# Kernel tuning notes

Measured on AMD Instinct MI355X. Metric: run time of the kernel, lower is better.

## Reference

```python
import jax, jax.numpy as jnp
import numpy as np
from jax import lax

NUM_QUBITS = 4
NUM_LAYERS = 2
EPS = 1e-5  # BatchNorm eps; eval mode with running_mean=0, running_var=1


def _cnot_ring_matrix():
    # CNOT(0,1); CNOT(1,2); CNOT(2,3); CNOT(3,0) as one 16x16 permutation.
    # PennyLane convention: wire 0 is the most-significant bit of the basis index.
    M = np.zeros((16, 16), dtype=np.complex64)
    for b in range(16):
        bb = b
        for cw, tw in [(0, 1), (1, 2), (2, 3), (3, 0)]:
            if (bb >> (3 - cw)) & 1:
                bb ^= 1 << (3 - tw)
        M[bb, b] = 1.0
    return M

CNOT_RING = jnp.asarray(_cnot_ring_matrix())
# ZSIGNS[w, b] = <b|Z_w|b> = +/-1
ZSIGNS = jnp.asarray(np.array([[1.0 - 2.0 * ((b >> (3 - w)) & 1) for b in range(16)]
                               for w in range(NUM_QUBITS)], dtype=np.float32))


def conv_bn_relu(x, w, b, gamma, beta):
    # Conv2d(k=3, pad=1) + BatchNorm2d (eval: mean=0, var=1) + ReLU, NCHW
    x = lax.conv_general_dilated(x, w, (1, 1), ((1, 1), (1, 1)),
                                 dimension_numbers=('NCHW', 'OIHW', 'NCHW'))
    x = x + b[None, :, None, None]
    x = gamma[None, :, None, None] * x * (1.0 / np.sqrt(1.0 + EPS)) + beta[None, :, None, None]
    return jax.nn.relu(x)


def maxpool2(x):
    return lax.reduce_window(x, -jnp.inf, lax.max, (1, 1, 2, 2), (1, 1, 2, 2), 'VALID')


def avgpool2(x):
    return lax.reduce_window(x, 0.0, lax.add, (1, 1, 2, 2), (1, 1, 2, 2), 'VALID') * 0.25


def quantum_layer(x, weights):
    # x: [B, 16] softmax outputs. Amplitude-encode (abs + L2 normalize), then
    # BasicEntanglerLayers (RX rotations + CNOT ring) x NUM_LAYERS, then <Z_i>.
    psi = jnp.abs(x)
    psi = psi / jnp.linalg.norm(psi, axis=1, keepdims=True)
    psi = psi.astype(jnp.complex64)  # [B, 16] batched statevectors
    for l in range(NUM_LAYERS):
        c = jnp.cos(weights[l] * 0.5).astype(jnp.complex64)
        s = jnp.sin(weights[l] * 0.5).astype(jnp.complex64)
        U = jnp.ones((1, 1), dtype=jnp.complex64)
        for q in range(NUM_QUBITS):
            g = jnp.stack([jnp.stack([c[q], -1j * s[q]]),
                           jnp.stack([-1j * s[q], c[q]])])  # RX(theta_q)
            U = jnp.kron(U, g)
        U = CNOT_RING @ U  # rotations first, then entangling ring
        psi = psi @ U.T    # batched apply: [B,16] x [16,16]
    probs = jnp.real(psi * jnp.conj(psi))  # [B, 16]
    return probs @ ZSIGNS.T                # [B, 4] Pauli-Z expvals


def setup_inputs() -> dict:
    key = jax.random.key(0)
    ks = jax.random.split(key, 16)
    B = 1024
    f32 = jnp.float32

    def w(k, shape, fan_in):
        return jax.random.normal(k, shape, dtype=f32) * np.float32(1.0 / np.sqrt(fan_in))

    inp = {
        'x': jax.random.normal(ks[0], (B, 3, 32, 32), dtype=f32),
        'conv1_w': w(ks[1], (32, 3, 3, 3), 3 * 9), 'conv1_b': jnp.zeros((32,), f32),
        'bn1_g': jnp.ones((32,), f32), 'bn1_b': jnp.zeros((32,), f32),
        'conv2_w': w(ks[2], (64, 32, 3, 3), 32 * 9), 'conv2_b': jnp.zeros((64,), f32),
        'bn2_g': jnp.ones((64,), f32), 'bn2_b': jnp.zeros((64,), f32),
        'conv3_w': w(ks[3], (128, 64, 3, 3), 64 * 9), 'conv3_b': jnp.zeros((128,), f32),
        'bn3_g': jnp.ones((128,), f32), 'bn3_b': jnp.zeros((128,), f32),
        'fr1_w': w(ks[4], (512, 2048), 2048), 'fr1_b': jnp.zeros((512,), f32),
        'fr2_w': w(ks[5], (16, 512), 512), 'fr2_b': jnp.zeros((16,), f32),
        'q_weights': jax.random.uniform(ks[6], (NUM_LAYERS, NUM_QUBITS), dtype=f32,
                                        minval=0.0, maxval=2.0 * np.pi),
        'h1_w': w(ks[7], (128, 4), 4), 'h1_b': jnp.zeros((128,), f32),
        'bnh_g': jnp.ones((128,), f32), 'bnh_b': jnp.zeros((128,), f32),
        'h2_w': w(ks[8], (100, 128), 128), 'h2_b': jnp.zeros((100,), f32),
    }
    return inp


def reference(x, conv1_w, conv1_b, bn1_g, bn1_b, conv2_w, conv2_b, bn2_g, bn2_b,
              conv3_w, conv3_b, bn3_g, bn3_b, fr1_w, fr1_b, fr2_w, fr2_b,
              q_weights, h1_w, h1_b, bnh_g, bnh_b, h2_w, h2_b):
    # classical_net (CIFAR100 branch)
    h = conv_bn_relu(x, conv1_w, conv1_b, bn1_g, bn1_b)
    h = maxpool2(h)                                   # [B,32,16,16]
    h = conv_bn_relu(h, conv2_w, conv2_b, bn2_g, bn2_b)
    h = maxpool2(h)                                   # [B,64,8,8]
    h = conv_bn_relu(h, conv3_w, conv3_b, bn3_g, bn3_b)  # [B,128,8,8]
    h = avgpool2(h)                                   # AdaptiveAvgPool2d((4,4)): 8->4
    h = h.reshape(h.shape[0], -1)                     # [B, 2048]
    # feature_reducer
    h = jax.nn.relu(h @ fr1_w.T + fr1_b)
    f = jax.nn.softmax(h @ fr2_w.T + fr2_b, axis=1)   # [B, 16]
    # quantum layer (batched 4-qubit statevector sim)
    q = quantum_layer(f, q_weights)                   # [B, 4]
    # head (BN eval-mode, Dropout inactive)
    y = q @ h1_w.T + h1_b
    y = bnh_g * y * (1.0 / np.sqrt(1.0 + EPS)) + bnh_b
    y = jax.nn.relu(y)
    return y @ h2_w.T + h2_b                          # [B, 100]
```

## Files before the change

kernel.cpp:

```cpp
#include <hip/hip_runtime.h>
#include <math.h>

#define NB 1024
static constexpr float BN_INV = 0.99999500003749975f;

typedef __attribute__((ext_vector_type(8))) short short8;
typedef __attribute__((ext_vector_type(4))) short s16x4;
typedef __attribute__((ext_vector_type(4))) float f32x4;

__device__ inline short f2bf(float f) {
  union { float f; unsigned u; } v;
  v.f = f;
  unsigned u = v.u;
  u += 0x7fff + ((u >> 16) & 1);
  return (short)(u >> 16);
}

__global__ void k_prepack(const float* __restrict__ c1w, const float* __restrict__ c1b,
                          const float* __restrict__ g1, const float* __restrict__ be1,
                          const float* __restrict__ c2w, const float* __restrict__ c2b,
                          const float* __restrict__ g2, const float* __restrict__ be2,
                          const float* __restrict__ c3w, const float* __restrict__ c3b,
                          const float* __restrict__ g3, const float* __restrict__ be3,
                          short* __restrict__ wp1, short* __restrict__ wp2,
                          short* __restrict__ wp3, float* __restrict__ scsh) {
  int i = blockIdx.x * 256 + threadIdx.x;
  int stride = gridDim.x * 256;
  for (int e = i; e < 2048; e += stride) {
    int j = e & 7, lane = (e >> 3) & 63, ct = (e >> 9) & 1, mf = e >> 10;
    int co = ct * 16 + (lane & 15), k = (lane >> 4) * 8 + j;
    int kx = (k >> 2) & 3, c = k & 3;
    float v = 0.f;
    if (mf == 0) {
      int ky = k >> 4;
      if (kx < 3 && c < 3) v = c1w[(co * 3 + c) * 9 + ky * 3 + kx] * g1[co] * BN_INV;
    } else {
      if (k < 16 && kx < 3 && c < 3)
        v = c1w[(co * 3 + c) * 9 + 6 + kx] * g1[co] * BN_INV;
    }
    wp1[e] = f2bf(v);
  }
  for (int e = i; e < 18432; e += stride) {
    int j = e & 7, lane = (e >> 3) & 63, ct = (e >> 9) & 3, off = e >> 11;
    int co = ct * 16 + (lane & 15), ci = (lane >> 4) * 8 + j;
    wp2[e] = f2bf(c2w[(co * 32 + ci) * 9 + off]);
  }
  for (int e = i; e < 73728; e += stride) {
    int j = e & 7, lane = (e >> 3) & 63, ct = (e >> 9) & 7, oh = e >> 12;
    int half = oh & 1, off = oh >> 1;
    int co = ct * 16 + (lane & 15), ci = half * 32 + (lane >> 4) * 8 + j;
    wp3[e] = f2bf(c3w[(co * 64 + ci) * 9 + off]);
  }
  if (i < 64) {
    float sc = g2[i] * BN_INV;
    scsh[i] = sc;
    scsh[64 + i] = sc * c2b[i] + be2[i];
  } else if (i < 192) {
    int c = i - 64;
    float sc = g3[c] * BN_INV;
    scsh[128 + c] = sc;
    scsh[256 + c] = sc * c3b[c] + be3[c];
  } else if (i < 224) {
    int c = i - 192;
    scsh[384 + c] = g1[c] * BN_INV * c1b[c] + be1[c];
  }
}

__global__ __launch_bounds__(256) void k_convfused(
    const float* __restrict__ x, const short* __restrict__ wp1,
    const short* __restrict__ wp2, const short* __restrict__ wp3,
    const float* __restrict__ scsh, const float* __restrict__ fr1w,
    short* __restrict__ wfr1, short* __restrict__ out3 ) {
  __shared__ __align__(16) char smem[40320];
  const int tid = threadIdx.x;
  const int bx = blockIdx.x;

  if (bx < 128) {
    int i = bx * 256 + tid;
    for (int e = i; e < 524288; e += 128 * 256) {
      float2 f = ((const float2*)fr1w)[e];
      unsigned lo = (unsigned)(unsigned short)f2bf(f.x);
      unsigned hi = (unsigned)(unsigned short)f2bf(f.y);
      ((unsigned*)wfr1)[e] = (hi << 16) | lo;
    }
    return;
  }

  short* inT = (short*)smem;
  short* tile1 = (short*)(smem + 25920);
  short* inT3 = (short*)(smem + 25920);

  const int b = bx - 128;
  const int wid = tid >> 6, lane = tid & 63, q = lane >> 4, n = lane & 15;

  const float* xb = x + b * 3072;
  f32x4 xf[3];
#pragma unroll
  for (int k = 0; k < 3; ++k) xf[k] = ((const f32x4*)xb)[tid + 256 * k];
  for (int i = tid; i < 1088; i += 256) {
    int cidx = i >> 4, w = i & 15, r, cc;
    if (cidx < 18) { r = 0; cc = cidx; }
    else if (cidx < 36) { r = 17; cc = cidx - 18; }
    else { int j = cidx - 36; r = 1 + (j >> 1); cc = (j & 1) * 17; }
    ((int*)&inT[(r * 18 + cc) * 40])[w] = 0;
  }
  for (int i = tid; i < 264; i += 256) {
    int cidx = i >> 1, w = i & 1, r, cc;
    if (cidx < 34) { r = 0; cc = cidx; }
    else if (cidx < 68) { r = 33; cc = cidx - 34; }
    else { int j = cidx - 68; r = 1 + (j >> 1); cc = (j & 1) * 33; }
    ((int*)&tile1[(r * 34 + cc) * 4])[w] = 0;
  }
  if (tid < 8) ((int*)tile1)[2312 + tid] = 0;
  __syncthreads();
#pragma unroll
  for (int k = 0; k < 3; ++k) {
    int e0 = (tid + 256 * k) * 4;
#pragma unroll
    for (int jj = 0; jj < 4; ++jj) {
      int e = e0 + jj;
      int c = e >> 10, rem = e & 1023, iy = rem >> 5, ix = rem & 31;
      tile1[((iy + 1) * 34 + (ix + 1)) * 4 + c] = f2bf(xf[k][jj]);
    }
  }
  __syncthreads();

  {
    const short8* wv1 = (const short8*)wp1;
    short8 a00 = wv1[0 * 64 + lane];
    short8 a01 = wv1[1 * 64 + lane];
    short8 a10 = wv1[2 * 64 + lane];
    short8 a11 = wv1[3 * 64 + lane];
    const int ky0 = q >> 1, kx0 = (q & 1) * 2;
    float sh1[2][4];
#pragma unroll
    for (int ct = 0; ct < 2; ++ct)
#pragma unroll
      for (int r = 0; r < 4; ++r) sh1[ct][r] = scsh[384 + ct * 16 + q * 4 + r];

#pragma unroll
    for (int h = 0; h < 2; ++h) {
      const int xb0 = h * 16 + n;
#pragma unroll
      for (int yh = 0; yh < 2; ++yh) {
        f32x4 acc[2][4];
#pragma unroll
        for (int ct = 0; ct < 2; ++ct)
#pragma unroll
          for (int yy = 0; yy < 4; ++yy) acc[ct][yy] = (f32x4)0.f;
#pragma unroll
        for (int yy = 0; yy < 4; ++yy) {
          int y = 8 * wid + yh * 4 + yy;
          const short* p0 = &tile1[((y + ky0) * 34 + xb0 + kx0) * 4];
          const short* p1 = &tile1[((y + 2) * 34 + xb0 + kx0) * 4];
          s16x4 b0l = *(const s16x4*)p0, b0h = *(const s16x4*)(p0 + 4);
          s16x4 b1l = *(const s16x4*)p1, b1h = *(const s16x4*)(p1 + 4);
          short8 B0 = __builtin_shufflevector(b0l, b0h, 0, 1, 2, 3, 4, 5, 6, 7);
          short8 B1 = __builtin_shufflevector(b1l, b1h, 0, 1, 2, 3, 4, 5, 6, 7);
          acc[0][yy] = __builtin_amdgcn_mfma_f32_16x16x32_bf16(a00, B0, acc[0][yy], 0, 0, 0);
          acc[0][yy] = __builtin_amdgcn_mfma_f32_16x16x32_bf16(a10, B1, acc[0][yy], 0, 0, 0);
          acc[1][yy] = __builtin_amdgcn_mfma_f32_16x16x32_bf16(a01, B0, acc[1][yy], 0, 0, 0);
          acc[1][yy] = __builtin_amdgcn_mfma_f32_16x16x32_bf16(a11, B1, acc[1][yy], 0, 0, 0);
        }
#pragma unroll
        for (int ct = 0; ct < 2; ++ct)
#pragma unroll
          for (int yp = 0; yp < 2; ++yp)
#pragma unroll
            for (int r = 0; r < 4; ++r) {
              float v0 = fmaxf(acc[ct][2 * yp][r] + sh1[ct][r], 0.f);
              float v1 = fmaxf(acc[ct][2 * yp + 1][r] + sh1[ct][r], 0.f);
              float m = fmaxf(v0, v1);
              m = fmaxf(m, __shfl_xor(m, 1));
              if ((n & 1) == 0) {
                int co = ct * 16 + q * 4 + r;
                int yq = 4 * wid + yh * 2 + yp, xq = 8 * h + (n >> 1);
                inT[((yq + 1) * 18 + (xq + 1)) * 40 + co] = f2bf(m);
              }
            }
      }
    }
  }
  __syncthreads();

  for (int i = tid; i < 1152; i += 256) {
    int cidx = i >> 5, w = i & 31, r, cc;
    if (cidx < 10) { r = 0; cc = cidx; }
    else if (cidx < 20) { r = 9; cc = cidx - 10; }
    else { int j = cidx - 20; r = 1 + (j >> 1); cc = (j & 1) * 9; }
    ((int*)&inT3[(r * 10 + cc) * 72])[w] = 0;
  }
  __syncthreads();

  {
    const short8* wv = (const short8*)wp2;
    f32x4 acc[4][4];
#pragma unroll
    for (int t = 0; t < 4; ++t)
#pragma unroll
      for (int ct = 0; ct < 4; ++ct) acc[t][ct] = (f32x4)0.f;

#pragma unroll
    for (int off = 0; off < 9; ++off) {
      const int ky = off / 3, kx = off % 3;
      short8 a[4];
#pragma unroll
      for (int ct = 0; ct < 4; ++ct) a[ct] = wv[(off * 4 + ct) * 64 + lane];
#pragma unroll
      for (int t = 0; t < 4; ++t) {
        int y = 4 * wid + t;
        short8 bf = *(const short8*)&inT[((y + ky) * 18 + (n + kx)) * 40 + q * 8];
#pragma unroll
        for (int ct = 0; ct < 4; ++ct)
          acc[t][ct] = __builtin_amdgcn_mfma_f32_16x16x32_bf16(a[ct], bf,
                                                               acc[t][ct], 0, 0, 0);
      }
    }

    const float* sc2 = scsh;
    const float* sh2 = scsh + 64;
#pragma unroll
    for (int ct = 0; ct < 4; ++ct) {
      float vm[4][4];
#pragma unroll
      for (int t = 0; t < 4; ++t)
#pragma unroll
        for (int r = 0; r < 4; ++r) {
          int co = ct * 16 + q * 4 + r;
          float v = fmaf(sc2[co], acc[t][ct][r], sh2[co]);
          v = fmaxf(v, 0.f);
          vm[t][r] = fmaxf(v, __shfl_xor(v, 1));
        }
#pragma unroll
      for (int pp = 0; pp < 2; ++pp)
#pragma unroll
        for (int r = 0; r < 4; ++r) {
          float m = fmaxf(vm[2 * pp][r], vm[2 * pp + 1][r]);
          if ((n & 1) == 0) {
            int co = ct * 16 + q * 4 + r;
            int y2 = 2 * wid + pp, x2 = n >> 1;
            inT3[((y2 + 1) * 10 + (x2 + 1)) * 72 + co] = f2bf(m);
          }
        }
    }
  }
  __syncthreads();

  {
    const short8* wv = (const short8*)wp3;
    f32x4 acc[4][2];
#pragma unroll
    for (int c = 0; c < 4; ++c)
#pragma unroll
      for (int tt = 0; tt < 2; ++tt) acc[c][tt] = (f32x4)0.f;

    const int ct0 = (wid >> 1) * 4;
    const int t0 = (wid & 1) * 2;
#pragma unroll
    for (int off = 0; off < 9; ++off) {
      const int ky = off / 3, kx = off % 3;
#pragma unroll
      for (int half = 0; half < 2; ++half) {
        short8 a[4];
#pragma unroll
        for (int c = 0; c < 4; ++c)
          a[c] = wv[((off * 2 + half) * 8 + ct0 + c) * 64 + lane];
#pragma unroll
        for (int tt = 0; tt < 2; ++tt) {
          int y = 2 * (t0 + tt) + (n >> 3), xx = n & 7;
          short8 bf = *(const short8*)&inT3[((y + ky) * 10 + (xx + kx)) * 72 +
                                            half * 32 + q * 8];
#pragma unroll
          for (int c = 0; c < 4; ++c)
            acc[c][tt] = __builtin_amdgcn_mfma_f32_16x16x32_bf16(a[c], bf,
                                                                 acc[c][tt], 0, 0, 0);
        }
      }
    }

    const float* sc3 = scsh + 128;
    const float* sh3 = scsh + 256;
#pragma unroll
    for (int c = 0; c < 4; ++c) {
      int ct = ct0 + c;
#pragma unroll
      for (int tt = 0; tt < 2; ++tt) {
        int t = t0 + tt;
#pragma unroll
        for (int r = 0; r < 4; ++r) {
          int co = ct * 16 + q * 4 + r;
          float v = fmaf(sc3[co], acc[c][tt][r], sh3[co]);
          v = fmaxf(v, 0.f);
          float s = v + __shfl_xor(v, 1);
          s += __shfl_xor(s, 8);
          if ((n & 9) == 0)
            out3[(size_t)b * 2048 + co * 16 + t * 4 + (n >> 1)] = f2bf(s * 0.25f);
        }
      }
    }
  }
}

__global__ __launch_bounds__(256) void k_fr1m(
    const short* __restrict__ A, const short* __restrict__ W,
    const float* __restrict__ bias, float* __restrict__ C) {
  __shared__ __align__(16) short As[2 * 2304];
  __shared__ __align__(16) short Bs[2 * 2304];
  const int m0 = blockIdx.x * 32;
  const int n0 = blockIdx.y * 32;
  const int tid = threadIdx.x;
  const int w = tid >> 6, lane = tid & 63, q = lane >> 4, n = lane & 15;
  const int mt = w >> 1, nt = w & 1;
  const int srow = tid >> 3, sc = tid & 7;

  f32x4 acc = (f32x4)0.f;
  const short* Ab = A + (size_t)(m0 + srow) * 2048 + sc * 8;
  const short* Wb = W + (size_t)(n0 + srow) * 2048 + sc * 8;

  short8 av = *(const short8*)Ab;
  short8 bv = *(const short8*)Wb;
  for (int it = 0; it < 32; ++it) {
    short* Asb = As + (it & 1) * 2304;
    short* Bsb = Bs + (it & 1) * 2304;
    *(short8*)&Asb[srow * 72 + sc * 8] = av;
    *(short8*)&Bsb[srow * 72 + sc * 8] = bv;
    if (it < 31) {
      av = *(const short8*)(Ab + (it + 1) * 64);
      bv = *(const short8*)(Wb + (it + 1) * 64);
    }
    __syncthreads();
#pragma unroll
    for (int kk = 0; kk < 2; ++kk) {
      short8 bfrag = *(const short8*)&Bsb[(nt * 16 + n) * 72 + kk * 32 + q * 8];
      short8 afrag = *(const short8*)&Asb[(mt * 16 + n) * 72 + kk * 32 + q * 8];
      acc = __builtin_amdgcn_mfma_f32_16x16x32_bf16(afrag, bfrag, acc, 0, 0, 0);
    }
  }
#pragma unroll
  for (int r = 0; r < 4; ++r) {
    int m = m0 + mt * 16 + q * 4 + r;
    int nn = n0 + nt * 16 + n;
    C[(size_t)m * 512 + nn] = fmaxf(acc[r] + bias[nn], 0.f);
  }
}

__global__ __launch_bounds__(64) void k_tail(
    const float* __restrict__ H, const float* __restrict__ W2,
    const float* __restrict__ b2, const float* __restrict__ qw,
    const float* __restrict__ h1w, const float* __restrict__ h1b,
    const float* __restrict__ bg, const float* __restrict__ bb,
    const float* __restrict__ h2w, const float* __restrict__ h2b,
    float* __restrict__ out) {
  __shared__ float hbuf[512];
  __shared__ float ybuf[128];
  const int b = blockIdx.x;
  const int lane = threadIdx.x;
  const float* hrow = H + b * 512;
  *(float4*)&hbuf[lane * 4] = *(const float4*)&hrow[lane * 4];
  *(float4*)&hbuf[256 + lane * 4] = *(const float4*)&hrow[256 + lane * 4];
  __syncthreads();

  const int j = lane & 15;
  const int grpk = lane >> 4;
  float partial = 0.f;
  const float* wrow = W2 + j * 512 + grpk * 128;
  const float* hb = hbuf + grpk * 128;
#pragma unroll
  for (int k = 0; k < 128; k += 4) {
    float4 wv = *(const float4*)&wrow[k];
    partial = fmaf(wv.x, hb[k + 0], partial);
    partial = fmaf(wv.y, hb[k + 1], partial);
    partial = fmaf(wv.z, hb[k + 2], partial);
    partial = fmaf(wv.w, hb[k + 3], partial);
  }
  partial += __shfl_xor(partial, 16);
  partial += __shfl_xor(partial, 32);
  float logit = partial + b2[j];

  float m = logit;
#pragma unroll
  for (int d = 1; d < 16; d <<= 1) m = fmaxf(m, __shfl_xor(m, d));
  float e = expf(logit - m);
  float s = e;
#pragma unroll
  for (int d = 1; d < 16; d <<= 1) s += __shfl_xor(s, d);
  float p = e / s;

  float n2 = p * p;
#pragma unroll
  for (int d = 1; d < 16; d <<= 1) n2 += __shfl_xor(n2, d);
  float amp = p / sqrtf(n2);
  float re = amp, im = 0.f;

#pragma unroll
  for (int l = 0; l < 2; ++l) {
#pragma unroll
    for (int q = 0; q < 4; ++q) {
      float th = qw[l * 4 + q] * 0.5f;
      float c = cosf(th), sn = sinf(th);
      int mask = 1 << (3 - q);
      float pre = __shfl_xor(re, mask);
      float pim = __shfl_xor(im, mask);
      float nre = fmaf(c, re, sn * pim);
      float nim = fmaf(c, im, -sn * pre);
      re = nre;
      im = nim;
    }
    int src = j;
    if (src & 1) src ^= 8;
    if (src & 2) src ^= 1;
    if (src & 4) src ^= 2;
    if (src & 8) src ^= 4;
    int srclane = (lane & 48) | src;
    re = __shfl(re, srclane);
    im = __shfl(im, srclane);
  }

  float prob = re * re + im * im;
  float qv[4];
#pragma unroll
  for (int w = 0; w < 4; ++w) {
    float sgn = ((j >> (3 - w)) & 1) ? -1.f : 1.f;
    float cwv = prob * sgn;
    cwv += __shfl_xor(cwv, 1);
    cwv += __shfl_xor(cwv, 2);
    cwv += __shfl_xor(cwv, 4);
    cwv += __shfl_xor(cwv, 8);
    qv[w] = cwv;
  }

#pragma unroll
  for (int t = 0; t < 2; ++t) {
    int jj = lane + 64 * t;
    float4 hw = *(const float4*)&h1w[jj * 4];
    float y = h1b[jj];
    y = fmaf(hw.x, qv[0], y);
    y = fmaf(hw.y, qv[1], y);
    y = fmaf(hw.z, qv[2], y);
    y = fmaf(hw.w, qv[3], y);
    y = fmaf(bg[jj] * BN_INV, y, bb[jj]);
    ybuf[jj] = fmaxf(y, 0.f);
  }
  __syncthreads();

#pragma unroll
  for (int t = 0; t < 2; ++t) {
    int k = lane + 64 * t;
    if (k < 100) {
      const float* wr = h2w + k * 128;
      float o = h2b[k];
#pragma unroll
      for (int jj = 0; jj < 128; jj += 4) {
        float4 wv = *(const float4*)&wr[jj];
        o = fmaf(wv.x, ybuf[jj + 0], o);
        o = fmaf(wv.y, ybuf[jj + 1], o);
        o = fmaf(wv.z, ybuf[jj + 2], o);
        o = fmaf(wv.w, ybuf[jj + 3], o);
      }
      out[b * 100 + k] = o;
    }
  }
}

extern "C" void kernel_launch(void* const* d_in, const int* in_sizes, int n_in,
                              void* d_out, int out_size, void* d_ws,
                              size_t ws_size, hipStream_t stream) {
  const float* x = (const float*)d_in[0];
  const float* c1w = (const float*)d_in[1];
  const float* c1b = (const float*)d_in[2];
  const float* g1 = (const float*)d_in[3];
  const float* be1 = (const float*)d_in[4];
  const float* c2w = (const float*)d_in[5];
  const float* c2b = (const float*)d_in[6];
  const float* g2 = (const float*)d_in[7];
  const float* be2 = (const float*)d_in[8];
  const float* c3w = (const float*)d_in[9];
  const float* c3b = (const float*)d_in[10];
  const float* g3 = (const float*)d_in[11];
  const float* be3 = (const float*)d_in[12];
  const float* fr1w = (const float*)d_in[13];
  const float* fr1b = (const float*)d_in[14];
  const float* fr2w = (const float*)d_in[15];
  const float* fr2b = (const float*)d_in[16];
  const float* qwts = (const float*)d_in[17];
  const float* h1w = (const float*)d_in[18];
  const float* h1b = (const float*)d_in[19];
  const float* bhg = (const float*)d_in[20];
  const float* bhb = (const float*)d_in[21];
  const float* h2w = (const float*)d_in[22];
  const float* h2b = (const float*)d_in[23];
  float* out = (float*)d_out;

  float* ws = (float*)d_ws;
  short* out3bf = (short*)ws;
  float* h1 = ws + 1048576;
  short* wfr1 = (short*)(ws + 1572864);
  short* wp2 = (short*)(ws + 2097152);
  short* wp3 = (short*)(ws + 2106368);
  float* scsh = ws + 2143232;
  short* wp1 = (short*)(ws + 2143744);

  k_prepack<<<96, 256, 0, stream>>>(c1w, c1b, g1, be1, c2w, c2b, g2, be2, c3w,
                                    c3b, g3, be3, wp1, wp2, wp3, scsh);
  k_convfused<<<NB + 128, 256, 0, stream>>>(x, wp1, wp2, wp3, scsh, fr1w, wfr1,
                                            out3bf);
  k_fr1m<<<dim3(32, 16), 256, 0, stream>>>(out3bf, wfr1, fr1b, h1);
  k_tail<<<NB, 64, 0, stream>>>(h1, fr2w, fr2b, qwts, h1w, h1b, bhg, bhb, h2w,
                                h2b, out);
}
```

Baseline: 178.2 us.

## Double fused conv block to 512 threads and split per-wave conv work

The fused conv kernel now runs with 512 threads (8 waves) per image instead of 256. Each wave handles half as many output rows or channel tiles in every conv stage. The conv3 input tile gets its own shared-memory region, so its halo can be zeroed up front and one barrier is dropped. The aim is more latency hiding and fewer serial MFMA chains per wave, paid for with more shared memory per block (49.6KB), which may reduce the number of blocks resident per CU.

```diff
diff --git a/kernel.cpp b/kernel.cpp
--- a/kernel.cpp
+++ b/kernel.cpp
@@ -66,18 +66,18 @@
   }
 }
 
-__global__ __launch_bounds__(256) void k_convfused(
+__global__ __launch_bounds__(512) void k_convfused(
     const float* __restrict__ x, const short* __restrict__ wp1,
     const short* __restrict__ wp2, const short* __restrict__ wp3,
     const float* __restrict__ scsh, const float* __restrict__ fr1w,
     short* __restrict__ wfr1, short* __restrict__ out3 ) {
-  __shared__ __align__(16) char smem[40320];
+  __shared__ __align__(16) char smem[49600];
   const int tid = threadIdx.x;
   const int bx = blockIdx.x;
 
   if (bx < 128) {
-    int i = bx * 256 + tid;
-    for (int e = i; e < 524288; e += 128 * 256) {
+    int i = bx * 512 + tid;
+    for (int e = i; e < 524288; e += 128 * 512) {
       float2 f = ((const float2*)fr1w)[e];
       unsigned lo = (unsigned)(unsigned short)f2bf(f.x);
       unsigned hi = (unsigned)(unsigned short)f2bf(f.y);
@@ -88,23 +88,23 @@
 
   short* inT = (short*)smem;
   short* tile1 = (short*)(smem + 25920);
-  short* inT3 = (short*)(smem + 25920);
+  short* inT3 = (short*)(smem + 35200);
 
   const int b = bx - 128;
   const int wid = tid >> 6, lane = tid & 63, q = lane >> 4, n = lane & 15;
 
   const float* xb = x + b * 3072;
-  f32x4 xf[3];
-#pragma unroll
-  for (int k = 0; k < 3; ++k) xf[k] = ((const f32x4*)xb)[tid + 256 * k];
-  for (int i = tid; i < 1088; i += 256) {
+  f32x4 xf0 = ((const f32x4*)xb)[tid];
+  f32x4 xf1;
+  if (tid < 256) xf1 = ((const f32x4*)xb)[tid + 512];
+  for (int i = tid; i < 1088; i += 512) {
     int cidx = i >> 4, w = i & 15, r, cc;
     if (cidx < 18) { r = 0; cc = cidx; }
     else if (cidx < 36) { r = 17; cc = cidx - 18; }
     else { int j = cidx - 36; r = 1 + (j >> 1); cc = (j & 1) * 17; }
     ((int*)&inT[(r * 18 + cc) * 40])[w] = 0;
   }
-  for (int i = tid; i < 264; i += 256) {
+  for (int i = tid; i < 264; i += 512) {
     int cidx = i >> 1, w = i & 1, r, cc;
     if (cidx < 34) { r = 0; cc = cidx; }
     else if (cidx < 68) { r = 33; cc = cidx - 34; }
@@ -112,15 +112,29 @@
     ((int*)&tile1[(r * 34 + cc) * 4])[w] = 0;
   }
   if (tid < 8) ((int*)tile1)[2312 + tid] = 0;
-  __syncthreads();
-#pragma unroll
-  for (int k = 0; k < 3; ++k) {
-    int e0 = (tid + 256 * k) * 4;
+  for (int i = tid; i < 1152; i += 512) {
+    int cidx = i >> 5, w = i & 31, r, cc;
+    if (cidx < 10) { r = 0; cc = cidx; }
+    else if (cidx < 20) { r = 9; cc = cidx - 10; }
+    else { int j = cidx - 20; r = 1 + (j >> 1); cc = (j & 1) * 9; }
+    ((int*)&inT3[(r * 10 + cc) * 72])[w] = 0;
+  }
+  {
+    int e0 = tid * 4;
 #pragma unroll
     for (int jj = 0; jj < 4; ++jj) {
       int e = e0 + jj;
       int c = e >> 10, rem = e & 1023, iy = rem >> 5, ix = rem & 31;
-      tile1[((iy + 1) * 34 + (ix + 1)) * 4 + c] = f2bf(xf[k][jj]);
+      tile1[((iy + 1) * 34 + (ix + 1)) * 4 + c] = f2bf(xf0[jj]);
+    }
+    if (tid < 256) {
+      int e1 = (tid + 512) * 4;
+#pragma unroll
+      for (int jj = 0; jj < 4; ++jj) {
+        int e = e1 + jj;
+        int c = e >> 10, rem = e & 1023, iy = rem >> 5, ix = rem & 31;
+        tile1[((iy + 1) * 34 + (ix + 1)) * 4 + c] = f2bf(xf1[jj]);
+      }
     }
   }
   __syncthreads();
@@ -141,62 +155,50 @@
 #pragma unroll
     for (int h = 0; h < 2; ++h) {
       const int xb0 = h * 16 + n;
-#pragma unroll
-      for (int yh = 0; yh < 2; ++yh) {
-        f32x4 acc[2][4];
-#pragma unroll
-        for (int ct = 0; ct < 2; ++ct)
-#pragma unroll
-          for (int yy = 0; yy < 4; ++yy) acc[ct][yy] = (f32x4)0.f;
-#pragma unroll
-        for (int yy = 0; yy < 4; ++yy) {
-          int y = 8 * wid + yh * 4 + yy;
-          const short* p0 = &tile1[((y + ky0) * 34 + xb0 + kx0) * 4];
-          const short* p1 = &tile1[((y + 2) * 34 + xb0 + kx0) * 4];
-          s16x4 b0l = *(const s16x4*)p0, b0h = *(const s16x4*)(p0 + 4);
-          s16x4 b1l = *(const s16x4*)p1, b1h = *(const s16x4*)(p1 + 4);
-          short8 B0 = __builtin_shufflevector(b0l, b0h, 0, 1, 2, 3, 4, 5, 6, 7);
-          short8 B1 = __builtin_shufflevector(b1l, b1h, 0, 1, 2, 3, 4, 5, 6, 7);
-          acc[0][yy] = __builtin_amdgcn_mfma_f32_16x16x32_bf16(a00, B0, acc[0][yy], 0, 0, 0);
-          acc[0][yy] = __builtin_amdgcn_mfma_f32_16x16x32_bf16(a10, B1, acc[0][yy], 0, 0, 0);
-          acc[1][yy] = __builtin_amdgcn_mfma_f32_16x16x32_bf16(a01, B0, acc[1][yy], 0, 0, 0);
-          acc[1][yy] = __builtin_amdgcn_mfma_f32_16x16x32_bf16(a11, B1, acc[1][yy], 0, 0, 0);
-        }
-#pragma unroll
-        for (int ct = 0; ct < 2; ++ct)
-#pragma unroll
-          for (int yp = 0; yp < 2; ++yp)
-#pragma unroll
-            for (int r = 0; r < 4; ++r) {
-              float v0 = fmaxf(acc[ct][2 * yp][r] + sh1[ct][r], 0.f);
-              float v1 = fmaxf(acc[ct][2 * yp + 1][r] + sh1[ct][r], 0.f);
-              float m = fmaxf(v0, v1);
-              m = fmaxf(m, __shfl_xor(m, 1));
-              if ((n & 1) == 0) {
-                int co = ct * 16 + q * 4 + r;
-                int yq = 4 * wid + yh * 2 + yp, xq = 8 * h + (n >> 1);
-                inT[((yq + 1) * 18 + (xq + 1)) * 40 + co] = f2bf(m);
-              }
+      f32x4 acc[2][4];
+#pragma unroll
+      for (int ct = 0; ct < 2; ++ct)
+#pragma unroll
+        for (int yy = 0; yy < 4; ++yy) acc[ct][yy] = (f32x4)0.f;
+#pragma unroll
+      for (int yy = 0; yy < 4; ++yy) {
+        int y = 4 * wid + yy;
+        const short* p0 = &tile1[((y + ky0) * 34 + xb0 + kx0) * 4];
+        const short* p1 = &tile1[((y + 2) * 34 + xb0 + kx0) * 4];
+        s16x4 b0l = *(const s16x4*)p0, b0h = *(const s16x4*)(p0 + 4);
+        s16x4 b1l = *(const s16x4*)p1, b1h = *(const s16x4*)(p1 + 4);
+        short8 B0 = __builtin_shufflevector(b0l, b0h, 0, 1, 2, 3, 4, 5, 6, 7);
+        short8 B1 = __builtin_shufflevector(b1l, b1h, 0, 1, 2, 3, 4, 5, 6, 7);
+        acc[0][yy] = __builtin_amdgcn_mfma_f32_16x16x32_bf16(a00, B0, acc[0][yy], 0, 0, 0);
+        acc[0][yy] = __builtin_amdgcn_mfma_f32_16x16x32_bf16(a10, B1, acc[0][yy], 0, 0, 0);
+        acc[1][yy] = __builtin_amdgcn_mfma_f32_16x16x32_bf16(a01, B0, acc[1][yy], 0, 0, 0);
+        acc[1][yy] = __builtin_amdgcn_mfma_f32_16x16x32_bf16(a11, B1, acc[1][yy], 0, 0, 0);
+      }
+#pragma unroll
+      for (int ct = 0; ct < 2; ++ct)
+#pragma unroll
+        for (int yp = 0; yp < 2; ++yp)
+#pragma unroll
+          for (int r = 0; r < 4; ++r) {
+            float v0 = fmaxf(acc[ct][2 * yp][r] + sh1[ct][r], 0.f);
+            float v1 = fmaxf(acc[ct][2 * yp + 1][r] + sh1[ct][r], 0.f);
+            float m = fmaxf(v0, v1);
+            m = fmaxf(m, __shfl_xor(m, 1));
+            if ((n & 1) == 0) {
+              int co = ct * 16 + q * 4 + r;
+              int yq = 2 * wid + yp, xq = 8 * h + (n >> 1);
+              inT[((yq + 1) * 18 + (xq + 1)) * 40 + co] = f2bf(m);
             }
-      }
-    }
-  }
-  __syncthreads();
-
-  for (int i = tid; i < 1152; i += 256) {
-    int cidx = i >> 5, w = i & 31, r, cc;
-    if (cidx < 10) { r = 0; cc = cidx; }
-    else if (cidx < 20) { r = 9; cc = cidx - 10; }
-    else { int j = cidx - 20; r = 1 + (j >> 1); cc = (j & 1) * 9; }
-    ((int*)&inT3[(r * 10 + cc) * 72])[w] = 0;
+          }
+    }
   }
   __syncthreads();
 
   {
     const short8* wv = (const short8*)wp2;
-    f32x4 acc[4][4];
-#pragma unroll
-    for (int t = 0; t < 4; ++t)
+    f32x4 acc[2][4];
+#pragma unroll
+    for (int t = 0; t < 2; ++t)
 #pragma unroll
       for (int ct = 0; ct < 4; ++ct) acc[t][ct] = (f32x4)0.f;
 
@@ -207,8 +209,8 @@
 #pragma unroll
       for (int ct = 0; ct < 4; ++ct) a[ct] = wv[(off * 4 + ct) * 64 + lane];
 #pragma unroll
-      for (int t = 0; t < 4; ++t) {
-        int y = 4 * wid + t;
+      for (int t = 0; t < 2; ++t) {
+        int y = 2 * wid + t;
         short8 bf = *(const short8*)&inT[((y + ky) * 18 + (n + kx)) * 40 + q * 8];
 #pragma unroll
         for (int ct = 0; ct < 4; ++ct)
@@ -220,50 +222,41 @@
     const float* sc2 = scsh;
     const float* sh2 = scsh + 64;
 #pragma unroll
-    for (int ct = 0; ct < 4; ++ct) {
-      float vm[4][4];
-#pragma unroll
-      for (int t = 0; t < 4; ++t)
-#pragma unroll
-        for (int r = 0; r < 4; ++r) {
-          int co = ct * 16 + q * 4 + r;
-          float v = fmaf(sc2[co], acc[t][ct][r], sh2[co]);
-          v = fmaxf(v, 0.f);
-          vm[t][r] = fmaxf(v, __shfl_xor(v, 1));
-        }
-#pragma unroll
-      for (int pp = 0; pp < 2; ++pp)
-#pragma unroll
-        for (int r = 0; r < 4; ++r) {
-          float m = fmaxf(vm[2 * pp][r], vm[2 * pp + 1][r]);
-          if ((n & 1) == 0) {
-            int co = ct * 16 + q * 4 + r;
-            int y2 = 2 * wid + pp, x2 = n >> 1;
-            inT3[((y2 + 1) * 10 + (x2 + 1)) * 72 + co] = f2bf(m);
-          }
-        }
-    }
+    for (int ct = 0; ct < 4; ++ct)
+#pragma unroll
+      for (int r = 0; r < 4; ++r) {
+        int co = ct * 16 + q * 4 + r;
+        float v0 = fmaf(sc2[co], acc[0][ct][r], sh2[co]);
+        float v1 = fmaf(sc2[co], acc[1][ct][r], sh2[co]);
+        v0 = fmaxf(v0, 0.f);
+        v1 = fmaxf(v1, 0.f);
+        float m0 = fmaxf(v0, __shfl_xor(v0, 1));
+        float m1 = fmaxf(v1, __shfl_xor(v1, 1));
+        float m = fmaxf(m0, m1);
+        if ((n & 1) == 0)
+          inT3[((wid + 1) * 10 + (n >> 1) + 1) * 72 + co] = f2bf(m);
+      }
   }
   __syncthreads();
 
   {
     const short8* wv = (const short8*)wp3;
-    f32x4 acc[4][2];
-#pragma unroll
-    for (int c = 0; c < 4; ++c)
+    f32x4 acc[2][2];
+#pragma unroll
+    for (int c = 0; c < 2; ++c)
 #pragma unroll
       for (int tt = 0; tt < 2; ++tt) acc[c][tt] = (f32x4)0.f;
 
-    const int ct0 = (wid >> 1) * 4;
+    const int ct0 = (wid >> 1) * 2;
     const int t0 = (wid & 1) * 2;
 #pragma unroll
     for (int off = 0; off < 9; ++off) {
       const int ky = off / 3, kx = off % 3;
 #pragma unroll
       for (int half = 0; half < 2; ++half) {
-        short8 a[4];
-#pragma unroll
-        for (int c = 0; c < 4; ++c)
+        short8 a[2];
+#pragma unroll
+        for (int c = 0; c < 2; ++c)
           a[c] = wv[((off * 2 + half) * 8 + ct0 + c) * 64 + lane];
 #pragma unroll
         for (int tt = 0; tt < 2; ++tt) {
@@ -271,7 +264,7 @@
           short8 bf = *(const short8*)&inT3[((y + ky) * 10 + (xx + kx)) * 72 +
                                             half * 32 + q * 8];
 #pragma unroll
-          for (int c = 0; c < 4; ++c)
+          for (int c = 0; c < 2; ++c)
             acc[c][tt] = __builtin_amdgcn_mfma_f32_16x16x32_bf16(a[c], bf,
                                                                  acc[c][tt], 0, 0, 0);
         }
@@ -281,7 +274,7 @@
     const float* sc3 = scsh + 128;
     const float* sh3 = scsh + 256;
 #pragma unroll
-    for (int c = 0; c < 4; ++c) {
+    for (int c = 0; c < 2; ++c) {
       int ct = ct0 + c;
 #pragma unroll
       for (int tt = 0; tt < 2; ++tt) {
@@ -502,7 +495,7 @@
 
   k_prepack<<<96, 256, 0, stream>>>(c1w, c1b, g1, be1, c2w, c2b, g2, be2, c3w,
                                     c3b, g3, be3, wp1, wp2, wp3, scsh);
-  k_convfused<<<NB + 128, 256, 0, stream>>>(x, wp1, wp2, wp3, scsh, fr1w, wfr1,
+  k_convfused<<<NB + 128, 512, 0, stream>>>(x, wp1, wp2, wp3, scsh, fr1w, wfr1,
                                             out3bf);
   k_fr1m<<<dim3(32, 16), 256, 0, stream>>>(out3bf, wfr1, fr1b, h1);
   k_tail<<<NB, 64, 0, stream>>>(h1, fr2w, fr2b, qwts, h1w, h1b, bhg, bhb, h2w,
```

Result: faster. 166.0 us (-6.8%).
